# Kernel optimization log

Measured on AMD Instinct MI355X. Metric: run time of the kernel, lower is better.

Reference implementation:

```python
import math
import jax, jax.numpy as jnp
import numpy as np
from jax import lax

B, H, W = 8, 96, 96
FC, R, P, KS, TOPK = 768, 12, 16, 13, 24
SUP_TH, SUP_MIX, OPEN_K, DIL, NMS = 0.28, 0.8, 3, 3, 3

# prototype anchor metadata (buffers, deterministic)
ORI = jnp.asarray(np.linspace(0.0, math.pi, P + 1)[:-1], jnp.float32)
_lenL = np.array([0.4, 0.7, 1.0, 1.25], np.float32)
_widL = np.array([0.12, 0.18, 0.24, 0.3], np.float32)
LEN = jnp.asarray(_lenL[np.arange(P) % 4])
WID = jnp.asarray(_widL[(np.arange(P) // 4) % 4])
_ax = np.linspace(-1.0, 1.0, KS).astype(np.float32)
_gy, _gx = np.meshgrid(_ax, _ax, indexing='ij')
GX, GY = jnp.asarray(_gx), jnp.asarray(_gy)


def conv2d(x, w, b, pad=0):
    y = lax.conv_general_dilated(x, w, (1, 1), [(pad, pad), (pad, pad)],
                                 dimension_numbers=('NCHW', 'OIHW', 'NCHW'))
    return y + b[None, :, None, None]


def maxpool(x, k):
    p = k // 2
    return lax.reduce_window(x, -jnp.inf, lax.max, (1, 1, k, k), (1, 1, 1, 1),
                             [(0, 0), (0, 0), (p, p), (p, p)])


def avgpool3(x):
    s = lax.reduce_window(x, 0.0, lax.add, (1, 1, 3, 3), (1, 1, 1, 1),
                          [(0, 0), (0, 0), (1, 1), (1, 1)])
    return s / 9.0  # torch count_include_pad=True


def normalize_map(t):
    mn = t.min(axis=(-2, -1), keepdims=True)
    mx = t.max(axis=(-2, -1), keepdims=True)
    return (t - mn) / jnp.maximum(mx - mn, 1e-6)


def binary_open(m, k):
    er = 1.0 - maxpool(1.0 - m, k)
    return jnp.clip(maxpool(er, k), 0.0, 1.0)


def support_mask_fn(carrier_hp, density):
    cs = normalize_map(avgpool3(jnp.abs(carrier_hp)))
    ds = normalize_map(density)
    ev = SUP_MIX * cs + (1.0 - SUP_MIX) * ds
    m = (ev >= SUP_TH).astype(carrier_hp.dtype)
    m = binary_open(m, OPEN_K)
    m = maxpool(m, DIL)
    return jnp.clip(m, 0.0, 1.0)


def setup_inputs() -> dict:
    key = jax.random.key(0)
    ks = jax.random.split(key, 16)
    d = {
        'features': jax.random.normal(ks[0], (B, FC, H, W), jnp.float32),
        'carrier_hp': jax.random.normal(ks[1], (B, 1, H, W), jnp.float32),
        'density': jax.random.uniform(ks[2], (B, 1, H, W), jnp.float32),
        # feature_project: 1x1 conv FC->R, 3x3 conv R->R
        'w1': jax.random.normal(ks[3], (R, FC, 1, 1), jnp.float32) * (1.0 / math.sqrt(FC)),
        'b1': jnp.zeros((R,), jnp.float32),
        'w2': jax.random.normal(ks[4], (R, R, 3, 3), jnp.float32) * (1.0 / math.sqrt(R * 9)),
        'b2': jnp.zeros((R,), jnp.float32),
        # post_mix: 1x1 conv (R+4)->R, 1x1 conv R->FC
        'w3': jax.random.normal(ks[5], (R, R + 4, 1, 1), jnp.float32) * (1.0 / math.sqrt(R + 4)),
        'b3': jnp.zeros((R,), jnp.float32),
        'w4': jax.random.normal(ks[6], (FC, R, 1, 1), jnp.float32) * (1.0 / math.sqrt(R)),
        'b4': jnp.zeros((FC,), jnp.float32),
        'proto': jax.random.normal(ks[7], (P, R), jnp.float32) * 0.02,
    }
    return d


def reference(features, carrier_hp, density, w1, b1, w2, b2, w3, b3, w4, b4, proto):
    gelu = lambda x: jax.nn.gelu(x, approximate=False)
    # 1) feature projection
    proj = gelu(conv2d(gelu(conv2d(features, w1, b1, 0)), w2, b2, 1))  # [B,R,H,W]
    # 2) occupancy + support
    occ = normalize_map(jnp.abs(proj).mean(axis=1, keepdims=True))      # [B,1,H,W]
    sup = support_mask_fn(carrier_hp, density)                          # [B,1,H,W]
    # 3) NMS + top-k anchors
    scores = occ * sup
    local_max = maxpool(scores, NMS)
    peak = ((scores >= local_max) & (scores > 0.05)).astype(scores.dtype)
    flat = (scores * peak).reshape(B, -1)
    vals, idx = lax.top_k(flat, TOPK)                                   # [B,K]
    anchor_map = jnp.zeros_like(flat).at[jnp.arange(B)[:, None], idx].set(vals)
    anchor_map = anchor_map.reshape(B, 1, H, W)
    ys, xs = idx // W, idx % W
    # 4) per-anchor prototype selection
    proj_flat = proj.reshape(B, R, H * W)
    feat_at = jnp.take_along_axis(proj_flat, jnp.broadcast_to(idx[:, None, :], (B, R, TOPK)), axis=2)  # [B,R,K]
    logits = jnp.einsum('brk,pr->bkp', feat_at, proto)
    pidx = jnp.argmax(logits, axis=-1)                                  # [B,K]
    ori, ln, wd = ORI[pidx], LEN[pidx], WID[pidx]
    # 5) oriented Gaussian footprints [B,K,KS,KS]
    c = jnp.cos(ori)[..., None, None]
    s = jnp.sin(ori)[..., None, None]
    xr = c * GX + s * GY
    yr = -s * GX + c * GY
    foot = jnp.exp(-(xr / ln[..., None, None]) ** 2 - (yr / wd[..., None, None]) ** 2)
    foot = foot * vals[..., None, None]
    emb = proto[pidx]                                                   # [B,K,R]
    contrib = emb[:, :, :, None, None] * foot[:, :, None]               # [B,K,R,KS,KS]
    # 6) scatter-stamp onto canvas
    off = jnp.arange(KS) - KS // 2
    yy = ys[:, :, None, None] + off[None, None, :, None]                # [B,K,KS,KS]
    xx = xs[:, :, None, None] + off[None, None, None, :]
    valid = ((yy >= 0) & (yy < H) & (xx >= 0) & (xx < W)).astype(contrib.dtype)
    yyc = jnp.clip(yy, 0, H - 1)
    xxc = jnp.clip(xx, 0, W - 1)

    def stamp(ctr, y2, x2, v):
        c0 = jnp.zeros((R, H, W), ctr.dtype)
        return c0.at[:, y2, x2].add(jnp.transpose(ctr, (1, 0, 2, 3)) * v[None])

    canvas = jax.vmap(stamp)(contrib, yyc, xxc, valid)                  # [B,R,H,W]
    # 7) support-lock + post mix
    canvas = canvas * sup
    extras = jnp.concatenate([occ, sup, anchor_map, normalize_map(density)], axis=1)
    mixed = conv2d(gelu(conv2d(jnp.concatenate([canvas, extras], axis=1), w3, b3, 0)), w4, b4, 0)
    return mixed
```

## Files before the change

kernel.cpp:

```cpp
#include <hip/hip_runtime.h>
#include <math.h>

#define Bn 8
#define Hh 96
#define Ww 96
#define NPIX 9216
#define FCn 768
#define Rr 12
#define Pp 16
#define KSn 13
#define TOPKn 24
#define CAPc 1536

__device__ __forceinline__ float gelu_f(float x) {
  return 0.5f * x * (1.0f + erff(x * 0.70710678118654752440f));
}

__global__ __launch_bounds__(256) void k_conv1_part(
    const float* __restrict__ feat, const float* __restrict__ w1,
    float* __restrict__ partial) {
  __shared__ float w1s[192 * 12];
  int s = blockIdx.x & 3;
  int pixblk = blockIdx.x >> 2;
  int c0 = s * 192;
  for (int i = threadIdx.x; i < 192 * 12; i += 256) {
    int c = i / 12, r = i % 12;
    w1s[i] = w1[r * FCn + c0 + c];
  }
  __syncthreads();
  int px0 = pixblk * 512 + threadIdx.x * 2;
  int b = px0 / NPIX, hw = px0 % NPIX;
  const float* fb = feat + (size_t)b * FCn * NPIX + (size_t)c0 * NPIX + hw;
  float acc0[12], acc1[12];
#pragma unroll
  for (int r = 0; r < 12; r++) { acc0[r] = 0.f; acc1[r] = 0.f; }
  for (int c = 0; c < 192; c += 4) {
    float2 f[4];
#pragma unroll
    for (int u = 0; u < 4; u++)
      f[u] = *(const float2*)(fb + (size_t)(c + u) * NPIX);
#pragma unroll
    for (int u = 0; u < 4; u++) {
#pragma unroll
      for (int r = 0; r < 12; r++) {
        float w = w1s[(c + u) * 12 + r];
        acc0[r] = fmaf(f[u].x, w, acc0[r]);
        acc1[r] = fmaf(f[u].y, w, acc1[r]);
      }
    }
  }
  float* outp = partial + (size_t)s * (Bn * Rr * NPIX) +
                (size_t)b * Rr * NPIX + hw;
#pragma unroll
  for (int r = 0; r < 12; r++)
    *(float2*)(outp + (size_t)r * NPIX) = make_float2(acc0[r], acc1[r]);
}

__global__ __launch_bounds__(256) void k_bias_gelu(
    const float* __restrict__ partial, const float* __restrict__ b1,
    float* __restrict__ t1, unsigned int* __restrict__ statsu) {
  int e4 = blockIdx.x * 256 + threadIdx.x;
  const int Q = (Bn * Rr * NPIX) / 4;
  const float4* pp = (const float4*)partial;
  float4 a = pp[e4], b_ = pp[e4 + Q], c = pp[e4 + 2 * Q], d = pp[e4 + 3 * Q];
  int r = (e4 / (NPIX / 4)) % Rr;
  float bias = b1[r];
  float4 v;
  v.x = gelu_f(((a.x + b_.x) + c.x) + d.x + bias);
  v.y = gelu_f(((a.y + b_.y) + c.y) + d.y + bias);
  v.z = gelu_f(((a.z + b_.z) + c.z) + d.z + bias);
  v.w = gelu_f(((a.w + b_.w) + c.w) + d.w + bias);
  ((float4*)t1)[e4] = v;
  if (e4 < 24) {
    statsu[e4 * 2 + 0] = 0x7f800000u;
    statsu[e4 * 2 + 1] = 0u;
  }
}

__global__ __launch_bounds__(256) void k_conv2(
    const float* __restrict__ t1, const float* __restrict__ w2,
    const float* __restrict__ b2, const float* __restrict__ carrier,
    const float* __restrict__ density, float* __restrict__ proj,
    float* __restrict__ occ_raw, float* __restrict__ cs_raw,
    unsigned int* __restrict__ statsu, float* __restrict__ canvas,
    float* __restrict__ anchor) {
  __shared__ float w2s[Rr * Rr * 9];
  __shared__ float b2s[Rr];
  for (int i = threadIdx.x; i < Rr * Rr * 9; i += 256) w2s[i] = w2[i];
  if (threadIdx.x < Rr) b2s[threadIdx.x] = b2[threadIdx.x];
  int pix = blockIdx.x * 256 + threadIdx.x;
  {
    float4 z = make_float4(0.f, 0.f, 0.f, 0.f);
    float4* c4 = (float4*)canvas;
#pragma unroll
    for (int q = 0; q < 3; q++) c4[(size_t)q * (Bn * NPIX) + pix] = z;
    anchor[pix] = 0.f;
  }
  __syncthreads();
  int b = pix / NPIX, hw = pix % NPIX;
  int y = hw / Ww, x = hw % Ww;
  float acc[12];
#pragma unroll
  for (int r = 0; r < 12; r++) acc[r] = 0.f;
  const float* tb = t1 + (size_t)b * Rr * NPIX;
  for (int ri = 0; ri < Rr; ri++) {
    const float* tc = tb + (size_t)ri * NPIX;
#pragma unroll
    for (int ky = 0; ky < 3; ky++) {
      int yy = y + ky - 1;
      if (yy < 0 || yy >= Hh) continue;
#pragma unroll
      for (int kx = 0; kx < 3; kx++) {
        int xx = x + kx - 1;
        if (xx < 0 || xx >= Ww) continue;
        float v = tc[yy * Ww + xx];
#pragma unroll
        for (int ro = 0; ro < 12; ro++)
          acc[ro] = fmaf(v, w2s[((ro * Rr + ri) * 3 + ky) * 3 + kx], acc[ro]);
      }
    }
  }
  float asum = 0.f;
  float* pb = proj + (size_t)b * Rr * NPIX + hw;
#pragma unroll
  for (int ro = 0; ro < 12; ro++) {
    float g = gelu_f(acc[ro] + b2s[ro]);
    pb[(size_t)ro * NPIX] = g;
    asum += fabsf(g);
  }
  float occv = asum / 12.0f;
  occ_raw[pix] = occv;

  const float* cb = carrier + (size_t)b * NPIX;
  float s9 = 0.f;
  for (int dy = -1; dy <= 1; dy++) {
    int yy = y + dy;
    if (yy < 0 || yy >= Hh) continue;
    for (int dx = -1; dx <= 1; dx++) {
      int xx = x + dx;
      if (xx < 0 || xx >= Ww) continue;
      s9 += fabsf(cb[yy * Ww + xx]);
    }
  }
  float csv = s9 / 9.0f;
  cs_raw[pix] = csv;
  float dv = density[pix];

  float mn0 = occv, mx0 = occv, mn1 = csv, mx1 = csv, mn2 = dv, mx2 = dv;
#pragma unroll
  for (int off = 32; off > 0; off >>= 1) {
    mn0 = fminf(mn0, __shfl_xor(mn0, off));
    mx0 = fmaxf(mx0, __shfl_xor(mx0, off));
    mn1 = fminf(mn1, __shfl_xor(mn1, off));
    mx1 = fmaxf(mx1, __shfl_xor(mx1, off));
    mn2 = fminf(mn2, __shfl_xor(mn2, off));
    mx2 = fmaxf(mx2, __shfl_xor(mx2, off));
  }
  if ((threadIdx.x & 63) == 0) {
    atomicMin(&statsu[(0 * Bn + b) * 2 + 0], __float_as_uint(mn0));
    atomicMax(&statsu[(0 * Bn + b) * 2 + 1], __float_as_uint(mx0));
    atomicMin(&statsu[(1 * Bn + b) * 2 + 0], __float_as_uint(mn1));
    atomicMax(&statsu[(1 * Bn + b) * 2 + 1], __float_as_uint(mx1));
    atomicMin(&statsu[(2 * Bn + b) * 2 + 0], __float_as_uint(mn2));
    atomicMax(&statsu[(2 * Bn + b) * 2 + 1], __float_as_uint(mx2));
  }
}

__global__ __launch_bounds__(1024) void k_support(
    const float* __restrict__ occ_raw, const float* __restrict__ cs_raw,
    const float* __restrict__ density, const float* __restrict__ stats,
    float* __restrict__ occ, float* __restrict__ ds, float* __restrict__ sup,
    float* __restrict__ scores) {
  __shared__ unsigned char mA[NPIX], mB[NPIX];
  int b = blockIdx.x;
  float omn = stats[(0 * Bn + b) * 2], omx = stats[(0 * Bn + b) * 2 + 1];
  float cmn = stats[(1 * Bn + b) * 2], cmx = stats[(1 * Bn + b) * 2 + 1];
  float dmn = stats[(2 * Bn + b) * 2], dmx = stats[(2 * Bn + b) * 2 + 1];
  float oiv = fmaxf(omx - omn, 1e-6f);
  float civ = fmaxf(cmx - cmn, 1e-6f);
  float div_ = fmaxf(dmx - dmn, 1e-6f);
  float occ9[9];
#pragma unroll
  for (int i = 0; i < 9; i++) {
    int p = threadIdx.x + i * 1024;
    float oc = (occ_raw[b * NPIX + p] - omn) / oiv;
    float cv = (cs_raw[b * NPIX + p] - cmn) / civ;
    float dv = (density[b * NPIX + p] - dmn) / div_;
    occ[b * NPIX + p] = oc;
    ds[b * NPIX + p] = dv;
    occ9[i] = oc;
    float ev = 0.8f * cv + 0.2f * dv;
    mA[p] = (ev >= 0.28f) ? 1 : 0;
  }
  __syncthreads();
#pragma unroll
  for (int i = 0; i < 9; i++) {
    int p = threadIdx.x + i * 1024;
    int y = p / Ww, x = p % Ww;
    unsigned char m = 1;
    for (int dy = -1; dy <= 1; dy++) {
      int yy = y + dy;
      if (yy < 0 || yy >= Hh) continue;
      for (int dx = -1; dx <= 1; dx++) {
        int xx = x + dx;
        if (xx < 0 || xx >= Ww) continue;
        m = (unsigned char)(m & mA[yy * Ww + xx]);
      }
    }
    mB[p] = m;
  }
  __syncthreads();
#pragma unroll
  for (int i = 0; i < 9; i++) {
    int p = threadIdx.x + i * 1024;
    int y = p / Ww, x = p % Ww;
    unsigned char m = 0;
    for (int dy = -1; dy <= 1; dy++) {
      int yy = y + dy;
      if (yy < 0 || yy >= Hh) continue;
      for (int dx = -1; dx <= 1; dx++) {
        int xx = x + dx;
        if (xx < 0 || xx >= Ww) continue;
        m = (unsigned char)(m | mB[yy * Ww + xx]);
      }
    }
    mA[p] = m;
  }
  __syncthreads();
#pragma unroll
  for (int i = 0; i < 9; i++) {
    int p = threadIdx.x + i * 1024;
    int y = p / Ww, x = p % Ww;
    unsigned char m = 0;
    for (int dy = -1; dy <= 1; dy++) {
      int yy = y + dy;
      if (yy < 0 || yy >= Hh) continue;
      for (int dx = -1; dx <= 1; dx++) {
        int xx = x + dx;
        if (xx < 0 || xx >= Ww) continue;
        m = (unsigned char)(m | mA[yy * Ww + xx]);
      }
    }
    float sv = (float)m;
    sup[b * NPIX + p] = sv;
    scores[b * NPIX + p] = occ9[i] * sv;
  }
}

__global__ __launch_bounds__(256) void k_topk(
    const float* __restrict__ scores, float* __restrict__ vals,
    int* __restrict__ idxs, float* __restrict__ anchor) {
  __shared__ float flat[NPIX];
  __shared__ float cval[CAPc];
  __shared__ int cidx[CAPc];
  __shared__ int cnt;
  __shared__ float rv[4];
  __shared__ int ri[4], rs[4];
  int b = blockIdx.x;
  const int tid = threadIdx.x;
  const int lane = tid & 63, wid = tid >> 6;
  const float* sc = scores + (size_t)b * NPIX;
#pragma unroll
  for (int i = 0; i < NPIX / 256; i++) flat[tid + i * 256] = sc[tid + i * 256];
  if (tid == 0) cnt = 0;
  __syncthreads();
  float pk[NPIX / 256];
#pragma unroll
  for (int i = 0; i < NPIX / 256; i++) {
    int p = tid + i * 256;
    int y = p / Ww, x = p % Ww;
    float s = flat[p];
    float lm = -INFINITY;
    for (int dy = -1; dy <= 1; dy++) {
      int yy = y + dy;
      if (yy < 0 || yy >= Hh) continue;
      for (int dx = -1; dx <= 1; dx++) {
        int xx = x + dx;
        if (xx < 0 || xx >= Ww) continue;
        lm = fmaxf(lm, flat[yy * Ww + xx]);
      }
    }
    pk[i] = (s >= lm && s > 0.05f) ? s : 0.0f;
  }
  __syncthreads();
#pragma unroll
  for (int i = 0; i < NPIX / 256; i++) {
    int p = tid + i * 256;
    flat[p] = pk[i];
    if (pk[i] > 0.f) {
      int slot = atomicAdd(&cnt, 1);
      if (slot < CAPc) {
        cval[slot] = pk[i];
        cidx[slot] = p;
      }
    }
  }
  __syncthreads();
  const int C = cnt;
  if (C <= CAPc) {
    for (int k = 0; k < TOPKn; k++) {
      float bv = -INFINITY;
      int bi = 0x7fffffff, bs = -1;
      for (int j = tid; j < C; j += 256) {
        float v = cval[j];
        int pi = cidx[j];
        if (v > bv || (v == bv && pi < bi)) {
          bv = v;
          bi = pi;
          bs = j;
        }
      }
      for (int off = 32; off > 0; off >>= 1) {
        float ov = __shfl_xor(bv, off);
        int oi = __shfl_xor(bi, off);
        int os = __shfl_xor(bs, off);
        if (ov > bv || (ov == bv && oi < bi)) {
          bv = ov;
          bi = oi;
          bs = os;
        }
      }
      if (lane == 0) {
        rv[wid] = bv;
        ri[wid] = bi;
        rs[wid] = bs;
      }
      __syncthreads();
      if (tid == 0) {
        float Bv = rv[0];
        int Bi = ri[0], Bs = rs[0];
        for (int w = 1; w < 4; w++) {
          if (rv[w] > Bv || (rv[w] == Bv && ri[w] < Bi)) {
            Bv = rv[w];
            Bi = ri[w];
            Bs = rs[w];
          }
        }
        if (Bv > 0.f) {
          vals[b * TOPKn + k] = Bv;
          idxs[b * TOPKn + k] = Bi;
          anchor[b * NPIX + Bi] = Bv;
          cval[Bs] = -INFINITY;
        } else {
          vals[b * TOPKn + k] = 0.f;
          idxs[b * TOPKn + k] = 0;
        }
      }
      __syncthreads();
    }
  } else {
    for (int k = 0; k < TOPKn; k++) {
      float bv = -INFINITY;
      int bi = 0x7fffffff;
      for (int p = tid; p < NPIX; p += 256) {
        float v = flat[p];
        if (v > bv || (v == bv && p < bi)) {
          bv = v;
          bi = p;
        }
      }
      for (int off = 32; off > 0; off >>= 1) {
        float ov = __shfl_xor(bv, off);
        int oi = __shfl_xor(bi, off);
        if (ov > bv || (ov == bv && oi < bi)) {
          bv = ov;
          bi = oi;
        }
      }
      if (lane == 0) {
        rv[wid] = bv;
        ri[wid] = bi;
      }
      __syncthreads();
      if (tid == 0) {
        float Bv = rv[0];
        int Bi = ri[0];
        for (int w = 1; w < 4; w++) {
          if (rv[w] > Bv || (rv[w] == Bv && ri[w] < Bi)) {
            Bv = rv[w];
            Bi = ri[w];
          }
        }
        if (Bv > 0.f) {
          vals[b * TOPKn + k] = Bv;
          idxs[b * TOPKn + k] = Bi;
          anchor[b * NPIX + Bi] = Bv;
          flat[Bi] = -INFINITY;
        } else {
          vals[b * TOPKn + k] = 0.f;
          idxs[b * TOPKn + k] = 0;
        }
      }
      __syncthreads();
    }
  }
}

__global__ __launch_bounds__(192) void k_stamp(
    const float* __restrict__ proj, const float* __restrict__ proto,
    const float* __restrict__ vals, const int* __restrict__ idxs,
    float* __restrict__ canvas) {
  int b = blockIdx.x / TOPKn, k = blockIdx.x % TOPKn;
  __shared__ float embs[12];
  __shared__ float prm[5];
  __shared__ int ppos[2];
  if (threadIdx.x == 0) {
    int id = idxs[b * TOPKn + k];
    float v = vals[b * TOPKn + k];
    float ft[12];
    for (int r = 0; r < 12; r++)
      ft[r] = proj[(size_t)(b * Rr + r) * NPIX + id];
    float bestL = -INFINITY;
    int bp = 0;
    for (int p = 0; p < Pp; p++) {
      float L = 0.f;
      for (int r = 0; r < 12; r++) L = fmaf(ft[r], proto[p * Rr + r], L);
      if (L > bestL) {
        bestL = L;
        bp = p;
      }
    }
    const float lenL[4] = {0.4f, 0.7f, 1.0f, 1.25f};
    const float widL[4] = {0.12f, 0.18f, 0.24f, 0.3f};
    float ori = (float)((M_PI / 16.0) * (double)bp);
    prm[0] = cosf(ori);
    prm[1] = sinf(ori);
    prm[2] = lenL[bp & 3];
    prm[3] = widL[(bp >> 2) & 3];
    prm[4] = v;
    ppos[0] = id / Ww;
    ppos[1] = id % Ww;
    for (int r = 0; r < 12; r++) embs[r] = proto[bp * Rr + r];
  }
  __syncthreads();
  float v = prm[4];
  if (v <= 0.f) return;
  int t = threadIdx.x;
  if (t >= KSn * KSn) return;
  int i = t / KSn, j = t % KSn;
  float gx = (float)(-1.0 + (double)j * (1.0 / 6.0));
  float gy = (float)(-1.0 + (double)i * (1.0 / 6.0));
  float c = prm[0], s = prm[1];
  float xr = c * gx + s * gy;
  float yr = -s * gx + c * gy;
  float tx = xr / prm[2], ty = yr / prm[3];
  float foot = expf(-(tx * tx) - (ty * ty)) * v;
  int yy = ppos[0] + i - KSn / 2;
  int xx = ppos[1] + j - KSn / 2;
  if (yy < 0 || yy >= Hh || xx < 0 || xx >= Ww) return;
  float* cp = canvas + (size_t)b * Rr * NPIX + yy * Ww + xx;
#pragma unroll
  for (int r = 0; r < 12; r++) atomicAdd(cp + (size_t)r * NPIX, embs[r] * foot);
}

__global__ __launch_bounds__(256) void k_post1(
    const float* __restrict__ canvas, const float* __restrict__ sup,
    const float* __restrict__ occ, const float* __restrict__ anchor,
    const float* __restrict__ ds, const float* __restrict__ w3,
    const float* __restrict__ b3, float* __restrict__ h) {
  __shared__ float w3s[12 * 16], b3s[12];
  for (int i = threadIdx.x; i < 192; i += 256) w3s[i] = w3[i];
  if (threadIdx.x < 12) b3s[threadIdx.x] = b3[threadIdx.x];
  __syncthreads();
  int pix = blockIdx.x * 256 + threadIdx.x;
  int b = pix / NPIX, hw = pix % NPIX;
  float in16[16];
  float sv = sup[pix];
#pragma unroll
  for (int r = 0; r < 12; r++)
    in16[r] = canvas[(size_t)(b * Rr + r) * NPIX + hw] * sv;
  in16[12] = occ[pix];
  in16[13] = sv;
  in16[14] = anchor[pix];
  in16[15] = ds[pix];
  float* hb = h + (size_t)b * Rr * NPIX + hw;
#pragma unroll
  for (int ro = 0; ro < 12; ro++) {
    float acc = 0.f;
#pragma unroll
    for (int ci = 0; ci < 16; ci++)
      acc = fmaf(in16[ci], w3s[ro * 16 + ci], acc);
    hb[(size_t)ro * NPIX] = gelu_f(acc + b3s[ro]);
  }
}

__global__ __launch_bounds__(256) void k_post2(
    const float* __restrict__ h, const float* __restrict__ w4,
    const float* __restrict__ b4, float* __restrict__ out) {
  __shared__ float w4s[16 * 12], b4s[16];
  int bx = blockIdx.x;
  int hwblk = bx % 9;
  int g = (bx / 9) % 48;
  int b = bx / (9 * 48);
  int oc0 = g * 16;
  for (int i = threadIdx.x; i < 192; i += 256) w4s[i] = w4[oc0 * 12 + i];
  if (threadIdx.x < 16) b4s[threadIdx.x] = b4[oc0 + threadIdx.x];
  __syncthreads();
  int hw = hwblk * 1024 + threadIdx.x * 4;
  const float* hb = h + (size_t)b * Rr * NPIX + hw;
  float4 hreg[12];
#pragma unroll
  for (int r = 0; r < 12; r++)
    hreg[r] = *(const float4*)(hb + (size_t)r * NPIX);
  float* ob = out + (size_t)(b * FCn + oc0) * NPIX + hw;
#pragma unroll
  for (int j = 0; j < 16; j++) {
    float ax = 0.f, ay = 0.f, az = 0.f, aw = 0.f;
#pragma unroll
    for (int r = 0; r < 12; r++) {
      float w = w4s[j * 12 + r];
      ax = fmaf(hreg[r].x, w, ax);
      ay = fmaf(hreg[r].y, w, ay);
      az = fmaf(hreg[r].z, w, az);
      aw = fmaf(hreg[r].w, w, aw);
    }
    float bb = b4s[j];
    *(float4*)(ob + (size_t)j * NPIX) =
        make_float4(ax + bb, ay + bb, az + bb, aw + bb);
  }
}

extern "C" void kernel_launch(void* const* d_in, const int* in_sizes, int n_in,
                              void* d_out, int out_size, void* d_ws,
                              size_t ws_size, hipStream_t stream) {
  const float* features = (const float*)d_in[0];
  const float* carrier = (const float*)d_in[1];
  const float* density = (const float*)d_in[2];
  const float* w1 = (const float*)d_in[3];
  const float* b1 = (const float*)d_in[4];
  const float* w2 = (const float*)d_in[5];
  const float* b2 = (const float*)d_in[6];
  const float* w3 = (const float*)d_in[7];
  const float* b3 = (const float*)d_in[8];
  const float* w4 = (const float*)d_in[9];
  const float* b4 = (const float*)d_in[10];
  const float* proto = (const float*)d_in[11];
  float* out = (float*)d_out;
  float* ws = (float*)d_ws;

  const size_t NT = (size_t)Bn * Rr * NPIX;
  float* t1 = ws;
  float* partial = ws + NT;
  float* proj = partial;
  float* canvas = partial + NT;
  float* h = partial + 2 * NT;
  float* sm = ws + 5 * NT;
  float* occ_raw = sm;
  float* cs_raw = sm + (size_t)Bn * NPIX;
  float* occ = sm + 2 * (size_t)Bn * NPIX;
  float* ds = sm + 3 * (size_t)Bn * NPIX;
  float* sup = sm + 4 * (size_t)Bn * NPIX;
  float* scores = sm + 5 * (size_t)Bn * NPIX;
  float* anchor = sm + 6 * (size_t)Bn * NPIX;
  float* stats = sm + 7 * (size_t)Bn * NPIX;
  unsigned int* statsu = (unsigned int*)stats;
  float* vals = stats + 64;
  int* idxs = (int*)(vals + Bn * TOPKn);

  k_conv1_part<<<144 * 4, 256, 0, stream>>>(features, w1, partial);
  k_bias_gelu<<<(int)(NT / 4 / 256), 256, 0, stream>>>(partial, b1, t1, statsu);
  k_conv2<<<288, 256, 0, stream>>>(t1, w2, b2, carrier, density, proj, occ_raw,
                                   cs_raw, statsu, canvas, anchor);
  k_support<<<Bn, 1024, 0, stream>>>(occ_raw, cs_raw, density, stats, occ, ds,
                                     sup, scores);
  k_topk<<<Bn, 256, 0, stream>>>(scores, vals, idxs, anchor);
  k_stamp<<<Bn * TOPKn, 192, 0, stream>>>(proj, proto, vals, idxs, canvas);
  k_post1<<<288, 256, 0, stream>>>(canvas, sup, occ, anchor, ds, w3, b3, h);
  k_post2<<<Bn * 48 * 9, 256, 0, stream>>>(h, w4, b4, out);
}
```

Measured before the change: 562.4 us.

## Split conv1 channel reduction eightfold and fuse support mask with top-k

```diff
diff --git a/kernel.cpp b/kernel.cpp
--- a/kernel.cpp
+++ b/kernel.cpp
@@ -11,6 +11,7 @@
 #define KSn 13
 #define TOPKn 24
 #define CAPc 1536
+#define NSPLIT 8
 
 __device__ __forceinline__ float gelu_f(float x) {
   return 0.5f * x * (1.0f + erff(x * 0.70710678118654752440f));
@@ -19,11 +20,11 @@
 __global__ __launch_bounds__(256) void k_conv1_part(
     const float* __restrict__ feat, const float* __restrict__ w1,
     float* __restrict__ partial) {
-  __shared__ float w1s[192 * 12];
-  int s = blockIdx.x & 3;
-  int pixblk = blockIdx.x >> 2;
-  int c0 = s * 192;
-  for (int i = threadIdx.x; i < 192 * 12; i += 256) {
+  __shared__ float w1s[96 * 12];
+  int s = blockIdx.x & 7;
+  int pixblk = blockIdx.x >> 3;
+  int c0 = s * 96;
+  for (int i = threadIdx.x; i < 96 * 12; i += 256) {
     int c = i / 12, r = i % 12;
     w1s[i] = w1[r * FCn + c0 + c];
   }
@@ -34,7 +35,7 @@
   float acc0[12], acc1[12];
 #pragma unroll
   for (int r = 0; r < 12; r++) { acc0[r] = 0.f; acc1[r] = 0.f; }
-  for (int c = 0; c < 192; c += 4) {
+  for (int c = 0; c < 96; c += 4) {
     float2 f[4];
 #pragma unroll
     for (int u = 0; u < 4; u++)
@@ -62,15 +63,20 @@
   int e4 = blockIdx.x * 256 + threadIdx.x;
   const int Q = (Bn * Rr * NPIX) / 4;
   const float4* pp = (const float4*)partial;
-  float4 a = pp[e4], b_ = pp[e4 + Q], c = pp[e4 + 2 * Q], d = pp[e4 + 3 * Q];
+  float4 v = pp[e4];
+#pragma unroll
+  for (int s = 1; s < NSPLIT; s++) {
+    float4 t = pp[e4 + s * Q];
+    v.x += t.x; v.y += t.y; v.z += t.z; v.w += t.w;
+  }
   int r = (e4 / (NPIX / 4)) % Rr;
   float bias = b1[r];
-  float4 v;
-  v.x = gelu_f(((a.x + b_.x) + c.x) + d.x + bias);
-  v.y = gelu_f(((a.y + b_.y) + c.y) + d.y + bias);
-  v.z = gelu_f(((a.z + b_.z) + c.z) + d.z + bias);
-  v.w = gelu_f(((a.w + b_.w) + c.w) + d.w + bias);
-  ((float4*)t1)[e4] = v;
+  float4 o;
+  o.x = gelu_f(v.x + bias);
+  o.y = gelu_f(v.y + bias);
+  o.z = gelu_f(v.z + bias);
+  o.w = gelu_f(v.w + bias);
+  ((float4*)t1)[e4] = o;
   if (e4 < 24) {
     statsu[e4 * 2 + 0] = 0x7f800000u;
     statsu[e4 * 2 + 1] = 0u;
@@ -166,23 +172,33 @@
   }
 }
 
-__global__ __launch_bounds__(1024) void k_support(
+__global__ __launch_bounds__(1024) void k_support_topk(
     const float* __restrict__ occ_raw, const float* __restrict__ cs_raw,
     const float* __restrict__ density, const float* __restrict__ stats,
     float* __restrict__ occ, float* __restrict__ ds, float* __restrict__ sup,
-    float* __restrict__ scores) {
+    float* __restrict__ vals, int* __restrict__ idxs,
+    float* __restrict__ anchor) {
   __shared__ unsigned char mA[NPIX], mB[NPIX];
+  __shared__ float flat[NPIX];
+  __shared__ float cval[CAPc];
+  __shared__ int cidx[CAPc];
+  __shared__ int cnt;
+  __shared__ float rv[16];
+  __shared__ int ri[16], rs[16];
   int b = blockIdx.x;
+  const int tid = threadIdx.x;
+  const int lane = tid & 63, wid = tid >> 6;
   float omn = stats[(0 * Bn + b) * 2], omx = stats[(0 * Bn + b) * 2 + 1];
   float cmn = stats[(1 * Bn + b) * 2], cmx = stats[(1 * Bn + b) * 2 + 1];
   float dmn = stats[(2 * Bn + b) * 2], dmx = stats[(2 * Bn + b) * 2 + 1];
   float oiv = fmaxf(omx - omn, 1e-6f);
   float civ = fmaxf(cmx - cmn, 1e-6f);
   float div_ = fmaxf(dmx - dmn, 1e-6f);
+  if (tid == 0) cnt = 0;
   float occ9[9];
 #pragma unroll
   for (int i = 0; i < 9; i++) {
-    int p = threadIdx.x + i * 1024;
+    int p = tid + i * 1024;
     float oc = (occ_raw[b * NPIX + p] - omn) / oiv;
     float cv = (cs_raw[b * NPIX + p] - cmn) / civ;
     float dv = (density[b * NPIX + p] - dmn) / div_;
@@ -195,7 +211,7 @@
   __syncthreads();
 #pragma unroll
   for (int i = 0; i < 9; i++) {
-    int p = threadIdx.x + i * 1024;
+    int p = tid + i * 1024;
     int y = p / Ww, x = p % Ww;
     unsigned char m = 1;
     for (int dy = -1; dy <= 1; dy++) {
@@ -212,7 +228,7 @@
   __syncthreads();
 #pragma unroll
   for (int i = 0; i < 9; i++) {
-    int p = threadIdx.x + i * 1024;
+    int p = tid + i * 1024;
     int y = p / Ww, x = p % Ww;
     unsigned char m = 0;
     for (int dy = -1; dy <= 1; dy++) {
@@ -229,7 +245,7 @@
   __syncthreads();
 #pragma unroll
   for (int i = 0; i < 9; i++) {
-    int p = threadIdx.x + i * 1024;
+    int p = tid + i * 1024;
     int y = p / Ww, x = p % Ww;
     unsigned char m = 0;
     for (int dy = -1; dy <= 1; dy++) {
@@ -243,31 +259,13 @@
     }
     float sv = (float)m;
     sup[b * NPIX + p] = sv;
-    scores[b * NPIX + p] = occ9[i] * sv;
-  }
-}
-
-__global__ __launch_bounds__(256) void k_topk(
-    const float* __restrict__ scores, float* __restrict__ vals,
-    int* __restrict__ idxs, float* __restrict__ anchor) {
-  __shared__ float flat[NPIX];
-  __shared__ float cval[CAPc];
-  __shared__ int cidx[CAPc];
-  __shared__ int cnt;
-  __shared__ float rv[4];
-  __shared__ int ri[4], rs[4];
-  int b = blockIdx.x;
-  const int tid = threadIdx.x;
-  const int lane = tid & 63, wid = tid >> 6;
-  const float* sc = scores + (size_t)b * NPIX;
-#pragma unroll
-  for (int i = 0; i < NPIX / 256; i++) flat[tid + i * 256] = sc[tid + i * 256];
-  if (tid == 0) cnt = 0;
-  __syncthreads();
-  float pk[NPIX / 256];
-#pragma unroll
-  for (int i = 0; i < NPIX / 256; i++) {
-    int p = tid + i * 256;
+    flat[p] = occ9[i] * sv;
+  }
+  __syncthreads();
+  float pk[9];
+#pragma unroll
+  for (int i = 0; i < 9; i++) {
+    int p = tid + i * 1024;
     int y = p / Ww, x = p % Ww;
     float s = flat[p];
     float lm = -INFINITY;
@@ -284,8 +282,8 @@
   }
   __syncthreads();
 #pragma unroll
-  for (int i = 0; i < NPIX / 256; i++) {
-    int p = tid + i * 256;
+  for (int i = 0; i < 9; i++) {
+    int p = tid + i * 1024;
     flat[p] = pk[i];
     if (pk[i] > 0.f) {
       int slot = atomicAdd(&cnt, 1);
@@ -301,7 +299,7 @@
     for (int k = 0; k < TOPKn; k++) {
       float bv = -INFINITY;
       int bi = 0x7fffffff, bs = -1;
-      for (int j = tid; j < C; j += 256) {
+      for (int j = tid; j < C; j += 1024) {
         float v = cval[j];
         int pi = cidx[j];
         if (v > bv || (v == bv && pi < bi)) {
@@ -329,7 +327,7 @@
       if (tid == 0) {
         float Bv = rv[0];
         int Bi = ri[0], Bs = rs[0];
-        for (int w = 1; w < 4; w++) {
+        for (int w = 1; w < 16; w++) {
           if (rv[w] > Bv || (rv[w] == Bv && ri[w] < Bi)) {
             Bv = rv[w];
             Bi = ri[w];
@@ -352,7 +350,7 @@
     for (int k = 0; k < TOPKn; k++) {
       float bv = -INFINITY;
       int bi = 0x7fffffff;
-      for (int p = tid; p < NPIX; p += 256) {
+      for (int p = tid; p < NPIX; p += 1024) {
         float v = flat[p];
         if (v > bv || (v == bv && p < bi)) {
           bv = v;
@@ -375,7 +373,7 @@
       if (tid == 0) {
         float Bv = rv[0];
         int Bi = ri[0];
-        for (int w = 1; w < 4; w++) {
+        for (int w = 1; w < 16; w++) {
           if (rv[w] > Bv || (rv[w] == Bv && ri[w] < Bi)) {
             Bv = rv[w];
             Bi = ri[w];
@@ -544,26 +542,24 @@
   float* proj = partial;
   float* canvas = partial + NT;
   float* h = partial + 2 * NT;
-  float* sm = ws + 5 * NT;
+  float* sm = ws + 9 * NT;
   float* occ_raw = sm;
   float* cs_raw = sm + (size_t)Bn * NPIX;
   float* occ = sm + 2 * (size_t)Bn * NPIX;
   float* ds = sm + 3 * (size_t)Bn * NPIX;
   float* sup = sm + 4 * (size_t)Bn * NPIX;
-  float* scores = sm + 5 * (size_t)Bn * NPIX;
-  float* anchor = sm + 6 * (size_t)Bn * NPIX;
-  float* stats = sm + 7 * (size_t)Bn * NPIX;
+  float* anchor = sm + 5 * (size_t)Bn * NPIX;
+  float* stats = sm + 6 * (size_t)Bn * NPIX;
   unsigned int* statsu = (unsigned int*)stats;
   float* vals = stats + 64;
   int* idxs = (int*)(vals + Bn * TOPKn);
 
-  k_conv1_part<<<144 * 4, 256, 0, stream>>>(features, w1, partial);
+  k_conv1_part<<<144 * NSPLIT, 256, 0, stream>>>(features, w1, partial);
   k_bias_gelu<<<(int)(NT / 4 / 256), 256, 0, stream>>>(partial, b1, t1, statsu);
   k_conv2<<<288, 256, 0, stream>>>(t1, w2, b2, carrier, density, proj, occ_raw,
                                    cs_raw, statsu, canvas, anchor);
-  k_support<<<Bn, 1024, 0, stream>>>(occ_raw, cs_raw, density, stats, occ, ds,
-                                     sup, scores);
-  k_topk<<<Bn, 256, 0, stream>>>(scores, vals, idxs, anchor);
+  k_support_topk<<<Bn, 1024, 0, stream>>>(occ_raw, cs_raw, density, stats, occ,
+                                          ds, sup, vals, idxs, anchor);
   k_stamp<<<Bn * TOPKn, 192, 0, stream>>>(proj, proto, vals, idxs, canvas);
   k_post1<<<288, 256, 0, stream>>>(canvas, sup, occ, anchor, ds, w3, b3, h);
   k_post2<<<Bn * 48 * 9, 256, 0, stream>>>(h, w4, b4, out);
```

New measurement: 577.6 us. 2.7% more time.

## Fuse split-K reduction and GELU into conv2 with shared-memory halo tiles

Applied to the files above, without the earlier changes.

```diff
diff --git a/kernel.cpp b/kernel.cpp
--- a/kernel.cpp
+++ b/kernel.cpp
@@ -11,6 +11,7 @@
 #define KSn 13
 #define TOPKn 24
 #define CAPc 1536
+#define NSPLIT 4
 
 __device__ __forceinline__ float gelu_f(float x) {
   return 0.5f * x * (1.0f + erff(x * 0.70710678118654752440f));
@@ -18,8 +19,12 @@
 
 __global__ __launch_bounds__(256) void k_conv1_part(
     const float* __restrict__ feat, const float* __restrict__ w1,
-    float* __restrict__ partial) {
+    float* __restrict__ partial, unsigned int* __restrict__ statsu) {
   __shared__ float w1s[192 * 12];
+  if (blockIdx.x == 0 && threadIdx.x < 24) {
+    statsu[threadIdx.x * 2 + 0] = 0x7f800000u;
+    statsu[threadIdx.x * 2 + 1] = 0u;
+  }
   int s = blockIdx.x & 3;
   int pixblk = blockIdx.x >> 2;
   int c0 = s * 192;
@@ -34,13 +39,13 @@
   float acc0[12], acc1[12];
 #pragma unroll
   for (int r = 0; r < 12; r++) { acc0[r] = 0.f; acc1[r] = 0.f; }
-  for (int c = 0; c < 192; c += 4) {
-    float2 f[4];
-#pragma unroll
-    for (int u = 0; u < 4; u++)
+  for (int c = 0; c < 192; c += 8) {
+    float2 f[8];
+#pragma unroll
+    for (int u = 0; u < 8; u++)
       f[u] = *(const float2*)(fb + (size_t)(c + u) * NPIX);
 #pragma unroll
-    for (int u = 0; u < 4; u++) {
+    for (int u = 0; u < 8; u++) {
 #pragma unroll
       for (int r = 0; r < 12; r++) {
         float w = w1s[(c + u) * 12 + r];
@@ -56,39 +61,28 @@
     *(float2*)(outp + (size_t)r * NPIX) = make_float2(acc0[r], acc1[r]);
 }
 
-__global__ __launch_bounds__(256) void k_bias_gelu(
+__global__ __launch_bounds__(256) void k_conv2(
     const float* __restrict__ partial, const float* __restrict__ b1,
-    float* __restrict__ t1, unsigned int* __restrict__ statsu) {
-  int e4 = blockIdx.x * 256 + threadIdx.x;
-  const int Q = (Bn * Rr * NPIX) / 4;
-  const float4* pp = (const float4*)partial;
-  float4 a = pp[e4], b_ = pp[e4 + Q], c = pp[e4 + 2 * Q], d = pp[e4 + 3 * Q];
-  int r = (e4 / (NPIX / 4)) % Rr;
-  float bias = b1[r];
-  float4 v;
-  v.x = gelu_f(((a.x + b_.x) + c.x) + d.x + bias);
-  v.y = gelu_f(((a.y + b_.y) + c.y) + d.y + bias);
-  v.z = gelu_f(((a.z + b_.z) + c.z) + d.z + bias);
-  v.w = gelu_f(((a.w + b_.w) + c.w) + d.w + bias);
-  ((float4*)t1)[e4] = v;
-  if (e4 < 24) {
-    statsu[e4 * 2 + 0] = 0x7f800000u;
-    statsu[e4 * 2 + 1] = 0u;
-  }
-}
-
-__global__ __launch_bounds__(256) void k_conv2(
-    const float* __restrict__ t1, const float* __restrict__ w2,
-    const float* __restrict__ b2, const float* __restrict__ carrier,
-    const float* __restrict__ density, float* __restrict__ proj,
-    float* __restrict__ occ_raw, float* __restrict__ cs_raw,
-    unsigned int* __restrict__ statsu, float* __restrict__ canvas,
-    float* __restrict__ anchor) {
+    const float* __restrict__ w2, const float* __restrict__ b2,
+    const float* __restrict__ carrier, const float* __restrict__ density,
+    float* __restrict__ proj, float* __restrict__ occ_raw,
+    float* __restrict__ cs_raw, unsigned int* __restrict__ statsu,
+    float* __restrict__ canvas, float* __restrict__ anchor) {
   __shared__ float w2s[Rr * Rr * 9];
   __shared__ float b2s[Rr];
-  for (int i = threadIdx.x; i < Rr * Rr * 9; i += 256) w2s[i] = w2[i];
-  if (threadIdx.x < Rr) b2s[threadIdx.x] = b2[threadIdx.x];
-  int pix = blockIdx.x * 256 + threadIdx.x;
+  __shared__ float ts[Rr][10][34];
+  const int tid = threadIdx.x;
+  const int PLN = Bn * Rr * NPIX;
+  int bx = blockIdx.x;
+  int b = bx / 36;
+  int tt = bx % 36;
+  int ty0 = (tt / 3) * 8;
+  int tx0 = (tt % 3) * 32;
+  for (int i = tid; i < Rr * Rr * 9; i += 256) w2s[i] = w2[i];
+  if (tid < Rr) b2s[tid] = b2[tid];
+  int lx = tid & 31, ly = tid >> 5;
+  int y = ty0 + ly, x = tx0 + lx;
+  int pix = b * NPIX + y * Ww + x;
   {
     float4 z = make_float4(0.f, 0.f, 0.f, 0.f);
     float4* c4 = (float4*)canvas;
@@ -96,24 +90,31 @@
     for (int q = 0; q < 3; q++) c4[(size_t)q * (Bn * NPIX) + pix] = z;
     anchor[pix] = 0.f;
   }
-  __syncthreads();
-  int b = pix / NPIX, hw = pix % NPIX;
-  int y = hw / Ww, x = hw % Ww;
+  for (int i = tid; i < Rr * 10 * 34; i += 256) {
+    int ch = i / 340, rem = i % 340;
+    int ry = rem / 34, rx = rem % 34;
+    int gy = ty0 + ry - 1, gx = tx0 + rx - 1;
+    float val = 0.f;
+    if (gy >= 0 && gy < Hh && gx >= 0 && gx < Ww) {
+      size_t off = (size_t)b * Rr * NPIX + (size_t)ch * NPIX + gy * Ww + gx;
+      float a = partial[off];
+      float bb = partial[off + PLN];
+      float cc = partial[off + 2 * (size_t)PLN];
+      float dd = partial[off + 3 * (size_t)PLN];
+      val = gelu_f(((a + bb) + cc) + dd + b1[ch]);
+    }
+    ts[ch][ry][rx] = val;
+  }
+  __syncthreads();
   float acc[12];
 #pragma unroll
   for (int r = 0; r < 12; r++) acc[r] = 0.f;
-  const float* tb = t1 + (size_t)b * Rr * NPIX;
   for (int ri = 0; ri < Rr; ri++) {
-    const float* tc = tb + (size_t)ri * NPIX;
 #pragma unroll
     for (int ky = 0; ky < 3; ky++) {
-      int yy = y + ky - 1;
-      if (yy < 0 || yy >= Hh) continue;
 #pragma unroll
       for (int kx = 0; kx < 3; kx++) {
-        int xx = x + kx - 1;
-        if (xx < 0 || xx >= Ww) continue;
-        float v = tc[yy * Ww + xx];
+        float v = ts[ri][ly + ky][lx + kx];
 #pragma unroll
         for (int ro = 0; ro < 12; ro++)
           acc[ro] = fmaf(v, w2s[((ro * Rr + ri) * 3 + ky) * 3 + kx], acc[ro]);
@@ -121,7 +122,7 @@
     }
   }
   float asum = 0.f;
-  float* pb = proj + (size_t)b * Rr * NPIX + hw;
+  float* pb = proj + (size_t)b * Rr * NPIX + y * Ww + x;
 #pragma unroll
   for (int ro = 0; ro < 12; ro++) {
     float g = gelu_f(acc[ro] + b2s[ro]);
@@ -156,7 +157,7 @@
     mn2 = fminf(mn2, __shfl_xor(mn2, off));
     mx2 = fmaxf(mx2, __shfl_xor(mx2, off));
   }
-  if ((threadIdx.x & 63) == 0) {
+  if ((tid & 63) == 0) {
     atomicMin(&statsu[(0 * Bn + b) * 2 + 0], __float_as_uint(mn0));
     atomicMax(&statsu[(0 * Bn + b) * 2 + 1], __float_as_uint(mx0));
     atomicMin(&statsu[(1 * Bn + b) * 2 + 0], __float_as_uint(mn1));
@@ -539,11 +540,9 @@
   float* ws = (float*)d_ws;
 
   const size_t NT = (size_t)Bn * Rr * NPIX;
-  float* t1 = ws;
+  float* proj = ws;
   float* partial = ws + NT;
-  float* proj = partial;
-  float* canvas = partial + NT;
-  float* h = partial + 2 * NT;
+  float* h = partial;
   float* sm = ws + 5 * NT;
   float* occ_raw = sm;
   float* cs_raw = sm + (size_t)Bn * NPIX;
@@ -556,11 +555,11 @@
   unsigned int* statsu = (unsigned int*)stats;
   float* vals = stats + 64;
   int* idxs = (int*)(vals + Bn * TOPKn);
-
-  k_conv1_part<<<144 * 4, 256, 0, stream>>>(features, w1, partial);
-  k_bias_gelu<<<(int)(NT / 4 / 256), 256, 0, stream>>>(partial, b1, t1, statsu);
-  k_conv2<<<288, 256, 0, stream>>>(t1, w2, b2, carrier, density, proj, occ_raw,
-                                   cs_raw, statsu, canvas, anchor);
+  float* canvas = sm + 8 * (size_t)Bn * NPIX;
+
+  k_conv1_part<<<144 * NSPLIT, 256, 0, stream>>>(features, w1, partial, statsu);
+  k_conv2<<<288, 256, 0, stream>>>(partial, b1, w2, b2, carrier, density, proj,
+                                   occ_raw, cs_raw, statsu, canvas, anchor);
   k_support<<<Bn, 1024, 0, stream>>>(occ_raw, cs_raw, density, stats, occ, ds,
                                      sup, scores);
   k_topk<<<Bn, 256, 0, stream>>>(scores, vals, idxs, anchor);
```

After: 710.5 us. +26.3%, slower.
